# Performance work log

Hardware: AMD Instinct MI355X
Metric: run time of the kernel (lower is better)

## Reference

```python
import jax, jax.numpy as jnp
import numpy as np

N_PEGS = 32      # 33 holes, one empty at start
N_ACTIONS = 132  # 33 positions * 4 moves


def _constants():
    # English peg-solitaire board: 7x7 cross, 33 holes; hole 0 is the center (3,3).
    moves = np.array([[-1, 0], [1, 0], [0, -1], [0, 1]], dtype=np.int64)
    cells = [(i, j) for i in range(7) for j in range(7) if (2 <= i <= 4) or (2 <= j <= 4)]
    cells.remove((3, 3))
    grid = np.array([(3, 3)] + cells, dtype=np.int64)          # (33, 2)
    p2i = {tuple(p): k for k, p in enumerate(grid)}
    pos_ids = np.repeat(np.arange(33), 4)                      # (132,)
    move_ids = np.tile(np.arange(4), 33)                       # (132,)
    apos = grid[pos_ids]                                       # (132, 2)
    amov = moves[move_ids]
    midp = apos + amov
    tgtp = apos + 2 * amov
    mid_idx = np.array([p2i.get(tuple(p), 0) for p in midp], dtype=np.int64)
    tgt_idx = np.array([p2i.get(tuple(p), 0) for p in tgtp], dtype=np.int64)
    oob = np.array([(tuple(m) not in p2i) or (tuple(t) not in p2i)
                    for m, t in zip(midp, tgtp)], dtype=bool)  # (132,)
    return dict(
        action_pos_ids=jnp.asarray(pos_ids, dtype=jnp.int32),
        action_mid_indices=jnp.asarray(mid_idx, dtype=jnp.int32),
        action_target_indices=jnp.asarray(tgt_idx, dtype=jnp.int32),
        oob_mask=jnp.asarray(oob),
        i_indices=jnp.asarray(grid[:, 0], dtype=jnp.int32),
        j_indices=jnp.asarray(grid[:, 1], dtype=jnp.int32),
    )


def setup_inputs() -> dict:
    key = jax.random.key(0)
    n = 262144
    k1, k2, k3, k4 = jax.random.split(key, 4)
    pegs = (jax.random.uniform(k1, (n, 33)) > 0.5).astype(jnp.float32)
    n_pegs = jax.random.randint(k2, (n,), 2, 32).astype(jnp.int32)
    done = jnp.zeros((n,), dtype=bool)
    total_reward = jax.random.uniform(k3, (n,), dtype=jnp.float32)
    actions = jax.random.randint(k4, (n,), 0, N_ACTIONS).astype(jnp.int32)
    inp = {"pegs": pegs, "n_pegs": n_pegs, "done": done,
           "total_reward": total_reward, "actions": actions}
    inp.update(_constants())
    return inp


def _feasible(pegs, done, action_pos_ids, action_mid_indices,
              action_target_indices, oob_mask):
    # (n, 132) boolean feasible-action mask
    mask = ~oob_mask[None, :]
    no_peg = pegs == 0.0
    mask = mask & ~no_peg[:, action_pos_ids]          # source must have a peg
    mask = mask & (pegs[:, action_mid_indices] > 0)   # mid must have a peg
    mask = mask & (pegs[:, action_target_indices] == 0)  # target must be empty
    return mask & ~done[:, None]


def reference(pegs, n_pegs, done, total_reward, actions,
              action_pos_ids, action_mid_indices, action_target_indices,
              oob_mask, i_indices, j_indices):
    n = pegs.shape[0]
    env = jnp.arange(n)
    pos = action_pos_ids[actions]
    mid = action_mid_indices[actions]
    tgt = action_target_indices[actions]
    # execute the jump (same write order as torch: pos<-0, mid<-0, target<-1)
    pegs = pegs.at[env, pos].set(0.0).at[env, mid].set(0.0).at[env, tgt].set(1.0)
    n_pegs = n_pegs - 1
    rewards = jnp.where(n_pegs == 1, 1.0, 1.0 / (N_PEGS - 1)).astype(jnp.float32)
    done_win = n_pegs == 1
    feasible = _feasible(pegs, done, action_pos_ids, action_mid_indices,
                         action_target_indices, oob_mask)
    done_new = done_win | ~feasible.any(axis=1)
    total_reward = total_reward + rewards
    # state: (n, 7, 7, 3)
    ch0 = jnp.zeros((n, 7, 7), dtype=pegs.dtype).at[:, i_indices, j_indices].set(pegs)
    npf = n_pegs.astype(jnp.float32)
    peg_ratio = (npf - 1.0) / (N_PEGS - 1)
    removed_ratio = (N_PEGS - npf) / (N_PEGS - 1)
    states = jnp.stack([
        ch0,
        jnp.broadcast_to(peg_ratio[:, None, None], (n, 7, 7)),
        jnp.broadcast_to(removed_ratio[:, None, None], (n, 7, 7)),
    ], axis=-1)
    return rewards, states, done_new, pegs, n_pegs, total_reward
```

## Files before the change

### kernel.cpp

```cpp
#include <hip/hip_runtime.h>


#define NTH 256
#define WPB 4
#define EPW 64

typedef float f32x4 __attribute__((ext_vector_type(4)));

__device__ constexpr int C2B[33] = {
    24,  2,  3,  4,  9, 10, 11, 14, 15, 16, 17, 18, 19, 20,
    21, 22, 23, 25, 26, 27, 28, 29, 30, 31, 32, 33, 34,
    37, 38, 39, 44, 45, 46};

constexpr unsigned long long MASK33 = (1ull << 33) - 1;

constexpr unsigned long long cross_mask() {
    unsigned long long b = 0;
    for (int i = 0; i < 7; ++i)
        for (int j = 0; j < 7; ++j)
            if ((i >= 2 && i <= 4) || (j >= 2 && j <= 4))
                b |= 1ull << (i * 7 + j);
    return b;
}
constexpr unsigned long long cols_le(int jmax) {
    unsigned long long b = 0;
    for (int i = 0; i < 7; ++i)
        for (int j = 0; j <= jmax; ++j) b |= 1ull << (i * 7 + j);
    return b;
}
constexpr unsigned long long cols_ge(int jmin) {
    unsigned long long b = 0;
    for (int i = 0; i < 7; ++i)
        for (int j = jmin; j < 7; ++j) b |= 1ull << (i * 7 + j);
    return b;
}
constexpr unsigned long long B_MASK = cross_mask();
constexpr unsigned long long C_LE4  = cols_le(4);
constexpr unsigned long long C_GE2  = cols_ge(2);

__device__ __forceinline__ void wave_lds_fence() {
    asm volatile("s_waitcnt lgkmcnt(0)" ::: "memory");
    __builtin_amdgcn_sched_barrier(0);
}

__global__ __launch_bounds__(NTH, 6) void peg_step(
    const float* __restrict__ pegs_in,
    const int* __restrict__ n_pegs_in,
    const unsigned char* __restrict__ done_in,
    const float* __restrict__ tot_rew_in,
    const int* __restrict__ actions,
    const int* __restrict__ pos_ids,
    const int* __restrict__ mid_idx,
    const int* __restrict__ tgt_idx,
    float* __restrict__ out,
    int n)
{
    __shared__ unsigned long long s_cm[WPB][EPW + 1];
    __shared__ unsigned long long s_bb[WPB][EPW];
    __shared__ float s_r1[WPB][EPW], s_r2[WPB][EPW];

    const int t    = threadIdx.x;
    const int w    = t >> 6;
    const int lane = t & 63;
    const int ew0  = blockIdx.x * (WPB * EPW) + w * EPW;
    const int e    = ew0 + lane;

    s_cm[w][lane] = 0ull;

    const f32x4* src = (const f32x4*)(pegs_in + (size_t)ew0 * 33);
    f32x4 r[8], r8;
    #pragma unroll
    for (int k = 0; k < 8; ++k) r[k] = src[lane + 64 * k];
    if (lane < 16) r8 = src[512 + lane];

    const int a         = actions[e];
    const int np_new    = n_pegs_in[e] - 1;
    const bool done_old = (done_in[e] != 0);
    const float tot     = tot_rew_in[e];
    const int p = pos_ids[a], m = mid_idx[a], g = tgt_idx[a];

    const float rw  = (np_new == 1) ? 1.0f : (1.0f / 31.0f);
    const float npf = (float)np_new;
    out[e]                   = rw;
    out[(size_t)182 * n + e] = npf;
    out[(size_t)183 * n + e] = tot + rw;

    {
        unsigned long long* cm = s_cm[w];
        #pragma unroll
        for (int k = 0; k < 8; ++k) {
            const int q   = lane + 64 * k;
            const int f   = q * 4;
            const int env = f / 33;
            const int c   = f - env * 33;
            const unsigned mm = (r[k][0] != 0.0f) | ((r[k][1] != 0.0f) << 1) |
                                ((r[k][2] != 0.0f) << 2) | ((r[k][3] != 0.0f) << 3);
            const unsigned long long full = (unsigned long long)mm << c;
            atomicOr(&cm[env], full & MASK33);
            const unsigned long long hi = full >> 33;
            if (hi) atomicOr(&cm[env + 1], hi);
        }
        if (lane < 16) {
            const int q   = 512 + lane;
            const int f   = q * 4;
            const int env = f / 33;
            const int c   = f - env * 33;
            const unsigned mm = (r8[0] != 0.0f) | ((r8[1] != 0.0f) << 1) |
                                ((r8[2] != 0.0f) << 2) | ((r8[3] != 0.0f) << 3);
            const unsigned long long full = (unsigned long long)mm << c;
            atomicOr(&cm[env], full & MASK33);
            const unsigned long long hi = full >> 33;
            if (hi) atomicOr(&cm[env + 1], hi);
        }
    }

    wave_lds_fence();

    unsigned long long cm = s_cm[w][lane];
    cm &= ~(1ull << p);
    cm &= ~(1ull << m);
    cm |=  (1ull << g);

    unsigned long long P = 0;
    #pragma unroll
    for (int c = 0; c < 33; ++c)
        P |= ((cm >> c) & 1ull) << C2B[c];

    const unsigned long long E = ~P & B_MASK;
    const unsigned long long feas =
        (P & (P >> 1) & (E >> 2)  & C_LE4) |
        (P & (P << 1) & (E << 2)  & C_GE2) |
        (P & (P >> 7) & (E >> 14))         |
        (P & (P << 7) & (E << 14));

    const bool dn = (np_new == 1) | done_old | (feas == 0ull);
    out[(size_t)148 * n + e] = dn ? 1.0f : 0.0f;

    s_cm[w][lane] = cm;
    s_bb[w][lane] = P;
    s_r1[w][lane] = (npf - 1.0f)  * (1.0f / 31.0f);
    s_r2[w][lane] = (32.0f - npf) * (1.0f / 31.0f);

    wave_lds_fence();

    {
        f32x4* dst = (f32x4*)(out + (size_t)149 * n + (size_t)ew0 * 33);
        #pragma unroll
        for (int k = 0; k < 9; ++k) {
            const int q = lane + 64 * k;
            if (k < 8 || lane < 16) {
                const int f   = q * 4;
                const int env = f / 33;
                const int c   = f - env * 33;
                const unsigned long long cat =
                    s_cm[w][env] | (s_cm[w][env + 1] << 33);
                f32x4 v;
                #pragma unroll
                for (int rr = 0; rr < 4; ++rr)
                    v[rr] = (float)((unsigned int)(cat >> (c + rr)) & 1u);
                dst[q] = v;
            }
        }
    }

    {
        f32x4* dst = (f32x4*)(out + (size_t)n + (size_t)ew0 * 147);
        const int total = EPW * 147 / 4;
        for (int q = lane; q < total; q += 64) {
            const int f4 = q * 4;
            int env = f4 / 147;
            int el  = f4 - env * 147;
            unsigned long long bb = s_bb[w][env];
            float r1 = s_r1[w][env], r2 = s_r2[w][env];
            f32x4 v;
            #pragma unroll
            for (int rr = 0; rr < 4; ++rr) {
                if (el == 147) {
                    el = 0; ++env;
                    bb = s_bb[w][env]; r1 = s_r1[w][env]; r2 = s_r2[w][env];
                }
                const int rc = el / 3;
                const int ch = el - rc * 3;
                v[rr] = (ch == 0) ? (float)((unsigned int)(bb >> rc) & 1u)
                                  : ((ch == 1) ? r1 : r2);
                ++el;
            }
            dst[q] = v;
        }
    }
}

extern "C" void kernel_launch(void* const* d_in, const int* in_sizes, int n_in,
                              void* d_out, int out_size, void* d_ws, size_t ws_size,
                              hipStream_t stream) {
    const float* pegs          = (const float*)d_in[0];
    const int* n_pegs          = (const int*)d_in[1];
    const unsigned char* done  = (const unsigned char*)d_in[2];
    const float* total_reward  = (const float*)d_in[3];
    const int* actions         = (const int*)d_in[4];
    const int* pos_ids         = (const int*)d_in[5];
    const int* mid_idx         = (const int*)d_in[6];
    const int* tgt_idx         = (const int*)d_in[7];
    float* out = (float*)d_out;

    int n = in_sizes[1];
    dim3 grid(n / (WPB * EPW)), block(NTH);
    hipLaunchKernelGGL(peg_step, grid, block, 0, stream,
                       pegs, n_pegs, done, total_reward, actions,
                       pos_ids, mid_idx, tgt_idx, out, n);
}
```

Measured before the change: 44.83 us.

## Split peg step into compute and streaming-store kernels via workspace

Splits the single kernel into two. The first reads pegs, computes feasibility and scalars, and writes the packed 33-bit board per environment to workspace. The second reads those bitmasks back and writes the large state and peg output arrays. This separates the read-heavy phase from the store-heavy phase so each can run at its own occupancy, with launch_bounds relaxed. It costs an extra launch and an extra workspace round trip, and the original fused kernel is kept as a fallback when workspace is too small.

```diff
diff --git a/kernel.cpp b/kernel.cpp
--- a/kernel.cpp
+++ b/kernel.cpp
@@ -43,7 +43,15 @@
     __builtin_amdgcn_sched_barrier(0);
 }
 
-__global__ __launch_bounds__(NTH, 6) void peg_step(
+__device__ __forceinline__ unsigned long long cm_to_grid(unsigned long long cm) {
+    unsigned long long P = 0;
+    #pragma unroll
+    for (int c = 0; c < 33; ++c)
+        P |= ((cm >> c) & 1ull) << C2B[c];
+    return P;
+}
+
+__global__ __launch_bounds__(NTH) void peg_compute(
     const float* __restrict__ pegs_in,
     const int* __restrict__ n_pegs_in,
     const unsigned char* __restrict__ done_in,
@@ -53,11 +61,10 @@
     const int* __restrict__ mid_idx,
     const int* __restrict__ tgt_idx,
     float* __restrict__ out,
+    unsigned long long* __restrict__ ws_cm,
     int n)
 {
     __shared__ unsigned long long s_cm[WPB][EPW + 1];
-    __shared__ unsigned long long s_bb[WPB][EPW];
-    __shared__ float s_r1[WPB][EPW], s_r2[WPB][EPW];
 
     const int t    = threadIdx.x;
     const int w    = t >> 6;
@@ -121,11 +128,7 @@
     cm &= ~(1ull << m);
     cm |=  (1ull << g);
 
-    unsigned long long P = 0;
-    #pragma unroll
-    for (int c = 0; c < 33; ++c)
-        P |= ((cm >> c) & 1ull) << C2B[c];
-
+    const unsigned long long P = cm_to_grid(cm);
     const unsigned long long E = ~P & B_MASK;
     const unsigned long long feas =
         (P & (P >> 1) & (E >> 2)  & C_LE4) |
@@ -136,8 +139,30 @@
     const bool dn = (np_new == 1) | done_old | (feas == 0ull);
     out[(size_t)148 * n + e] = dn ? 1.0f : 0.0f;
 
+    ws_cm[e] = cm;
+}
+
+__global__ __launch_bounds__(NTH) void peg_stream(
+    const unsigned long long* __restrict__ ws_cm,
+    const float* __restrict__ npf_src,
+    float* __restrict__ out,
+    int n)
+{
+    __shared__ unsigned long long s_cm[WPB][EPW + 1];
+    __shared__ unsigned long long s_bb[WPB][EPW];
+    __shared__ float s_r1[WPB][EPW], s_r2[WPB][EPW];
+
+    const int t    = threadIdx.x;
+    const int w    = t >> 6;
+    const int lane = t & 63;
+    const int ew0  = blockIdx.x * (WPB * EPW) + w * EPW;
+    const int e    = ew0 + lane;
+
+    const unsigned long long cm = ws_cm[e];
+    const float npf = npf_src[e];
+
     s_cm[w][lane] = cm;
-    s_bb[w][lane] = P;
+    s_bb[w][lane] = cm_to_grid(cm);
     s_r1[w][lane] = (npf - 1.0f)  * (1.0f / 31.0f);
     s_r2[w][lane] = (32.0f - npf) * (1.0f / 31.0f);
 
@@ -190,6 +215,148 @@
     }
 }
 
+__global__ __launch_bounds__(NTH) void peg_mono(
+    const float* __restrict__ pegs_in,
+    const int* __restrict__ n_pegs_in,
+    const unsigned char* __restrict__ done_in,
+    const float* __restrict__ tot_rew_in,
+    const int* __restrict__ actions,
+    const int* __restrict__ pos_ids,
+    const int* __restrict__ mid_idx,
+    const int* __restrict__ tgt_idx,
+    float* __restrict__ out,
+    int n)
+{
+    __shared__ unsigned long long s_cm[WPB][EPW + 1];
+    __shared__ unsigned long long s_bb[WPB][EPW];
+    __shared__ float s_r1[WPB][EPW], s_r2[WPB][EPW];
+
+    const int t    = threadIdx.x;
+    const int w    = t >> 6;
+    const int lane = t & 63;
+    const int ew0  = blockIdx.x * (WPB * EPW) + w * EPW;
+    const int e    = ew0 + lane;
+
+    s_cm[w][lane] = 0ull;
+
+    const f32x4* src = (const f32x4*)(pegs_in + (size_t)ew0 * 33);
+    f32x4 r[8], r8;
+    #pragma unroll
+    for (int k = 0; k < 8; ++k) r[k] = src[lane + 64 * k];
+    if (lane < 16) r8 = src[512 + lane];
+
+    const int a         = actions[e];
+    const int np_new    = n_pegs_in[e] - 1;
+    const bool done_old = (done_in[e] != 0);
+    const float tot     = tot_rew_in[e];
+    const int p = pos_ids[a], m = mid_idx[a], g = tgt_idx[a];
+
+    const float rw  = (np_new == 1) ? 1.0f : (1.0f / 31.0f);
+    const float npf = (float)np_new;
+    out[e]                   = rw;
+    out[(size_t)182 * n + e] = npf;
+    out[(size_t)183 * n + e] = tot + rw;
+
+    {
+        unsigned long long* cm = s_cm[w];
+        #pragma unroll
+        for (int k = 0; k < 8; ++k) {
+            const int q   = lane + 64 * k;
+            const int f   = q * 4;
+            const int env = f / 33;
+            const int c   = f - env * 33;
+            const unsigned mm = (r[k][0] != 0.0f) | ((r[k][1] != 0.0f) << 1) |
+                                ((r[k][2] != 0.0f) << 2) | ((r[k][3] != 0.0f) << 3);
+            const unsigned long long full = (unsigned long long)mm << c;
+            atomicOr(&cm[env], full & MASK33);
+            const unsigned long long hi = full >> 33;
+            if (hi) atomicOr(&cm[env + 1], hi);
+        }
+        if (lane < 16) {
+            const int q   = 512 + lane;
+            const int f   = q * 4;
+            const int env = f / 33;
+            const int c   = f - env * 33;
+            const unsigned mm = (r8[0] != 0.0f) | ((r8[1] != 0.0f) << 1) |
+                                ((r8[2] != 0.0f) << 2) | ((r8[3] != 0.0f) << 3);
+            const unsigned long long full = (unsigned long long)mm << c;
+            atomicOr(&cm[env], full & MASK33);
+            const unsigned long long hi = full >> 33;
+            if (hi) atomicOr(&cm[env + 1], hi);
+        }
+    }
+
+    wave_lds_fence();
+
+    unsigned long long cm = s_cm[w][lane];
+    cm &= ~(1ull << p);
+    cm &= ~(1ull << m);
+    cm |=  (1ull << g);
+
+    const unsigned long long P = cm_to_grid(cm);
+    const unsigned long long E = ~P & B_MASK;
+    const unsigned long long feas =
+        (P & (P >> 1) & (E >> 2)  & C_LE4) |
+        (P & (P << 1) & (E << 2)  & C_GE2) |
+        (P & (P >> 7) & (E >> 14))         |
+        (P & (P << 7) & (E << 14));
+
+    const bool dn = (np_new == 1) | done_old | (feas == 0ull);
+    out[(size_t)148 * n + e] = dn ? 1.0f : 0.0f;
+
+    s_cm[w][lane] = cm;
+    s_bb[w][lane] = P;
+    s_r1[w][lane] = (npf - 1.0f)  * (1.0f / 31.0f);
+    s_r2[w][lane] = (32.0f - npf) * (1.0f / 31.0f);
+
+    wave_lds_fence();
+
+    {
+        f32x4* dst = (f32x4*)(out + (size_t)149 * n + (size_t)ew0 * 33);
+        #pragma unroll
+        for (int k = 0; k < 9; ++k) {
+            const int q = lane + 64 * k;
+            if (k < 8 || lane < 16) {
+                const int f   = q * 4;
+                const int env = f / 33;
+                const int c   = f - env * 33;
+                const unsigned long long cat =
+                    s_cm[w][env] | (s_cm[w][env + 1] << 33);
+                f32x4 v;
+                #pragma unroll
+                for (int rr = 0; rr < 4; ++rr)
+                    v[rr] = (float)((unsigned int)(cat >> (c + rr)) & 1u);
+                dst[q] = v;
+            }
+        }
+    }
+    {
+        f32x4* dst = (f32x4*)(out + (size_t)n + (size_t)ew0 * 147);
+        const int total = EPW * 147 / 4;
+        for (int q = lane; q < total; q += 64) {
+            const int f4 = q * 4;
+            int env = f4 / 147;
+            int el  = f4 - env * 147;
+            unsigned long long bb = s_bb[w][env];
+            float r1 = s_r1[w][env], r2 = s_r2[w][env];
+            f32x4 v;
+            #pragma unroll
+            for (int rr = 0; rr < 4; ++rr) {
+                if (el == 147) {
+                    el = 0; ++env;
+                    bb = s_bb[w][env]; r1 = s_r1[w][env]; r2 = s_r2[w][env];
+                }
+                const int rc = el / 3;
+                const int ch = el - rc * 3;
+                v[rr] = (ch == 0) ? (float)((unsigned int)(bb >> rc) & 1u)
+                                  : ((ch == 1) ? r1 : r2);
+                ++el;
+            }
+            dst[q] = v;
+        }
+    }
+}
+
 extern "C" void kernel_launch(void* const* d_in, const int* in_sizes, int n_in,
                               void* d_out, int out_size, void* d_ws, size_t ws_size,
                               hipStream_t stream) {
@@ -205,7 +372,17 @@
 
     int n = in_sizes[1];
     dim3 grid(n / (WPB * EPW)), block(NTH);
-    hipLaunchKernelGGL(peg_step, grid, block, 0, stream,
-                       pegs, n_pegs, done, total_reward, actions,
-                       pos_ids, mid_idx, tgt_idx, out, n);
-}
+
+    if (ws_size >= (size_t)n * 8) {
+        unsigned long long* ws_cm = (unsigned long long*)d_ws;
+        hipLaunchKernelGGL(peg_compute, grid, block, 0, stream,
+                           pegs, n_pegs, done, total_reward, actions,
+                           pos_ids, mid_idx, tgt_idx, out, ws_cm, n);
+        hipLaunchKernelGGL(peg_stream, grid, block, 0, stream,
+                           ws_cm, out + (size_t)182 * n, out, n);
+    } else {
+        hipLaunchKernelGGL(peg_mono, grid, block, 0, stream,
+                           pegs, n_pegs, done, total_reward, actions,
+                           pos_ids, mid_idx, tgt_idx, out, n);
+    }
+}
```

Measured after the change: 48.32 us. +7.8%, slower.

## Process two tiles per wave with both tiles' loads issued up front

Applied to the files above, without the earlier changes.

Each wave now handles two 64-environment tiles and issues the global loads for both before processing either. The grid shrinks to half as many blocks. The point is to put more memory requests in flight per wave and hide load latency behind the first tile's processing. In exchange, register pressure rises because both tiles' data is held at once, and the occupancy hint was removed from launch_bounds.

```diff
diff --git a/kernel.cpp b/kernel.cpp
--- a/kernel.cpp
+++ b/kernel.cpp
@@ -4,6 +4,7 @@
 #define NTH 256
 #define WPB 4
 #define EPW 64
+#define TPW 2
 
 typedef float f32x4 __attribute__((ext_vector_type(4)));
 
@@ -43,7 +44,24 @@
     __builtin_amdgcn_sched_barrier(0);
 }
 
-__global__ __launch_bounds__(NTH, 6) void peg_step(
+__device__ __forceinline__ unsigned long long cm_to_grid(unsigned long long cm) {
+    unsigned long long P = 0;
+    #pragma unroll
+    for (int c = 0; c < 33; ++c)
+        P |= ((cm >> c) & 1ull) << C2B[c];
+    return P;
+}
+
+struct TileRegs {
+    f32x4 r[8];
+    f32x4 r8;
+    int a, np_new, p, m, g;
+    bool done_old;
+    float tot;
+};
+
+__device__ __forceinline__ void load_tile(
+    TileRegs& T, int ew0, int lane,
     const float* __restrict__ pegs_in,
     const int* __restrict__ n_pegs_in,
     const unsigned char* __restrict__ done_in,
@@ -51,39 +69,36 @@
     const int* __restrict__ actions,
     const int* __restrict__ pos_ids,
     const int* __restrict__ mid_idx,
-    const int* __restrict__ tgt_idx,
-    float* __restrict__ out,
-    int n)
+    const int* __restrict__ tgt_idx)
 {
-    __shared__ unsigned long long s_cm[WPB][EPW + 1];
-    __shared__ unsigned long long s_bb[WPB][EPW];
-    __shared__ float s_r1[WPB][EPW], s_r2[WPB][EPW];
-
-    const int t    = threadIdx.x;
-    const int w    = t >> 6;
-    const int lane = t & 63;
-    const int ew0  = blockIdx.x * (WPB * EPW) + w * EPW;
-    const int e    = ew0 + lane;
+    const f32x4* src = (const f32x4*)(pegs_in + (size_t)ew0 * 33);
+    #pragma unroll
+    for (int k = 0; k < 8; ++k) T.r[k] = src[lane + 64 * k];
+    if (lane < 16) T.r8 = src[512 + lane];
+    const int e = ew0 + lane;
+    T.a        = actions[e];
+    T.np_new   = n_pegs_in[e] - 1;
+    T.done_old = (done_in[e] != 0);
+    T.tot      = tot_rew_in[e];
+    T.p = pos_ids[T.a]; T.m = mid_idx[T.a]; T.g = tgt_idx[T.a];
+}
+
+__device__ __forceinline__ void process_tile(
+    const TileRegs& T, int ew0, int lane, int w,
+    unsigned long long (*s_cm)[EPW + 1],
+    unsigned long long (*s_bb)[EPW],
+    float (*s_r1)[EPW], float (*s_r2)[EPW],
+    float* __restrict__ out, int n)
+{
+    const int e = ew0 + lane;
 
     s_cm[w][lane] = 0ull;
 
-    const f32x4* src = (const f32x4*)(pegs_in + (size_t)ew0 * 33);
-    f32x4 r[8], r8;
-    #pragma unroll
-    for (int k = 0; k < 8; ++k) r[k] = src[lane + 64 * k];
-    if (lane < 16) r8 = src[512 + lane];
-
-    const int a         = actions[e];
-    const int np_new    = n_pegs_in[e] - 1;
-    const bool done_old = (done_in[e] != 0);
-    const float tot     = tot_rew_in[e];
-    const int p = pos_ids[a], m = mid_idx[a], g = tgt_idx[a];
-
-    const float rw  = (np_new == 1) ? 1.0f : (1.0f / 31.0f);
-    const float npf = (float)np_new;
+    const float rw  = (T.np_new == 1) ? 1.0f : (1.0f / 31.0f);
+    const float npf = (float)T.np_new;
     out[e]                   = rw;
     out[(size_t)182 * n + e] = npf;
-    out[(size_t)183 * n + e] = tot + rw;
+    out[(size_t)183 * n + e] = T.tot + rw;
 
     {
         unsigned long long* cm = s_cm[w];
@@ -93,8 +108,8 @@
             const int f   = q * 4;
             const int env = f / 33;
             const int c   = f - env * 33;
-            const unsigned mm = (r[k][0] != 0.0f) | ((r[k][1] != 0.0f) << 1) |
-                                ((r[k][2] != 0.0f) << 2) | ((r[k][3] != 0.0f) << 3);
+            const unsigned mm = (T.r[k][0] != 0.0f) | ((T.r[k][1] != 0.0f) << 1) |
+                                ((T.r[k][2] != 0.0f) << 2) | ((T.r[k][3] != 0.0f) << 3);
             const unsigned long long full = (unsigned long long)mm << c;
             atomicOr(&cm[env], full & MASK33);
             const unsigned long long hi = full >> 33;
@@ -105,8 +120,8 @@
             const int f   = q * 4;
             const int env = f / 33;
             const int c   = f - env * 33;
-            const unsigned mm = (r8[0] != 0.0f) | ((r8[1] != 0.0f) << 1) |
-                                ((r8[2] != 0.0f) << 2) | ((r8[3] != 0.0f) << 3);
+            const unsigned mm = (T.r8[0] != 0.0f) | ((T.r8[1] != 0.0f) << 1) |
+                                ((T.r8[2] != 0.0f) << 2) | ((T.r8[3] != 0.0f) << 3);
             const unsigned long long full = (unsigned long long)mm << c;
             atomicOr(&cm[env], full & MASK33);
             const unsigned long long hi = full >> 33;
@@ -117,15 +132,11 @@
     wave_lds_fence();
 
     unsigned long long cm = s_cm[w][lane];
-    cm &= ~(1ull << p);
-    cm &= ~(1ull << m);
-    cm |=  (1ull << g);
-
-    unsigned long long P = 0;
-    #pragma unroll
-    for (int c = 0; c < 33; ++c)
-        P |= ((cm >> c) & 1ull) << C2B[c];
-
+    cm &= ~(1ull << T.p);
+    cm &= ~(1ull << T.m);
+    cm |=  (1ull << T.g);
+
+    const unsigned long long P = cm_to_grid(cm);
     const unsigned long long E = ~P & B_MASK;
     const unsigned long long feas =
         (P & (P >> 1) & (E >> 2)  & C_LE4) |
@@ -133,7 +144,7 @@
         (P & (P >> 7) & (E >> 14))         |
         (P & (P << 7) & (E << 14));
 
-    const bool dn = (np_new == 1) | done_old | (feas == 0ull);
+    const bool dn = (T.np_new == 1) | T.done_old | (feas == 0ull);
     out[(size_t)148 * n + e] = dn ? 1.0f : 0.0f;
 
     s_cm[w][lane] = cm;
@@ -190,6 +201,38 @@
     }
 }
 
+__global__ __launch_bounds__(NTH) void peg_step(
+    const float* __restrict__ pegs_in,
+    const int* __restrict__ n_pegs_in,
+    const unsigned char* __restrict__ done_in,
+    const float* __restrict__ tot_rew_in,
+    const int* __restrict__ actions,
+    const int* __restrict__ pos_ids,
+    const int* __restrict__ mid_idx,
+    const int* __restrict__ tgt_idx,
+    float* __restrict__ out,
+    int n)
+{
+    __shared__ unsigned long long s_cm[WPB][EPW + 1];
+    __shared__ unsigned long long s_bb[WPB][EPW];
+    __shared__ float s_r1[WPB][EPW], s_r2[WPB][EPW];
+
+    const int t    = threadIdx.x;
+    const int w    = t >> 6;
+    const int lane = t & 63;
+    const int ewA  = (blockIdx.x * WPB + w) * (TPW * EPW);
+    const int ewB  = ewA + EPW;
+
+    TileRegs A, B;
+    load_tile(A, ewA, lane, pegs_in, n_pegs_in, done_in, tot_rew_in,
+              actions, pos_ids, mid_idx, tgt_idx);
+    load_tile(B, ewB, lane, pegs_in, n_pegs_in, done_in, tot_rew_in,
+              actions, pos_ids, mid_idx, tgt_idx);
+
+    process_tile(A, ewA, lane, w, s_cm, s_bb, s_r1, s_r2, out, n);
+    process_tile(B, ewB, lane, w, s_cm, s_bb, s_r1, s_r2, out, n);
+}
+
 extern "C" void kernel_launch(void* const* d_in, const int* in_sizes, int n_in,
                               void* d_out, int out_size, void* d_ws, size_t ws_size,
                               hipStream_t stream) {
@@ -204,7 +247,7 @@
     float* out = (float*)d_out;
 
     int n = in_sizes[1];
-    dim3 grid(n / (WPB * EPW)), block(NTH);
+    dim3 grid(n / (WPB * EPW * TPW)), block(NTH);
     hipLaunchKernelGGL(peg_step, grid, block, 0, stream,
                        pegs, n_pegs, done, total_reward, actions,
                        pos_ids, mid_idx, tgt_idx, out, n);
```

Result: slower. 47.28 us (+5.5%).
